# Kernel optimization log

Measured on AMD Instinct MI355X. Metric: run time of the kernel, lower is better.

Reference implementation:

```python
import jax, jax.numpy as jnp
import numpy as np

VAR_FLOOR = 0.002
BS, A, IN, H, L, NNH, ATT, NACT = 1024, 32, 96, 64, 16, 64, 32, 16


def _lin(x, w, b):
    return x @ w.T + b


def _lrelu(x):
    return jax.nn.leaky_relu(x, 0.01)


def setup_inputs() -> dict:
    key = jax.random.key(0)
    ks = jax.random.split(key, 24)
    def w(k, o, i):
        return jax.random.normal(k, (o, i), jnp.float32) / np.float32(np.sqrt(i))
    def b(k, o):
        return jax.random.normal(k, (o,), jnp.float32) * 0.01
    N = BS * A
    return {
        "inputs": jax.random.normal(ks[0], (N, IN), jnp.float32),
        "hidden_state": jax.random.normal(ks[1], (N, H), jnp.float32),
        "eps": jax.random.normal(ks[2], (N, A * L), jnp.float32),
        "fc1_w": w(ks[3], H, IN), "fc1_b": b(ks[4], H),
        "gru_wih": w(ks[5], 3 * H, H), "gru_whh": w(ks[6], 3 * H, H),
        "gru_bih": b(ks[7], 3 * H), "gru_bhh": b(ks[8], 3 * H),
        "fc2_w": w(ks[9], NACT, H), "fc2_b": b(ks[10], NACT),
        "emb_w1": w(ks[11], NNH, H), "emb_b1": b(ks[12], NNH),
        "bn_g": jnp.ones((NNH,), jnp.float32), "bn_b": jnp.zeros((NNH,), jnp.float32),
        "emb_w2": w(ks[13], A * L * 2, NNH), "emb_b2": b(ks[14], A * L * 2),
        "msg_w1": w(ks[15], NNH, H + L), "msg_b1": b(ks[16], NNH),
        "msg_w2": w(ks[17], NACT, NNH), "msg_b2": b(ks[18], NACT),
        "wq_w": w(ks[19], ATT, H), "wq_b": b(ks[20], ATT),
        "wk_w": w(ks[21], ATT, L), "wk_b": b(ks[22], ATT),
        "bs": BS, "t": 0,
    }


def reference(inputs, hidden_state, eps, fc1_w, fc1_b, gru_wih, gru_whh, gru_bih,
              gru_bhh, fc2_w, fc2_b, emb_w1, emb_b1, bn_g, bn_b, emb_w2, emb_b2,
              msg_w1, msg_b1, msg_w2, msg_b2, wq_w, wq_b, wk_w, wk_b, bs, t):
    Hd = fc1_w.shape[0]
    x = jax.nn.relu(_lin(inputs, fc1_w, fc1_b))
    h_in = hidden_state.reshape(-1, Hd)
    # GRUCell
    gi = _lin(x, gru_wih, gru_bih)
    gh = _lin(h_in, gru_whh, gru_bhh)
    ir, iz, inn = jnp.split(gi, 3, axis=-1)
    hr, hz, hn = jnp.split(gh, 3, axis=-1)
    r = jax.nn.sigmoid(ir + hr)
    z = jax.nn.sigmoid(iz + hz)
    n = jnp.tanh(inn + r * hn)
    h = (1.0 - z) * n + z * h_in
    q = _lin(h, fc2_w, fc2_b)
    # embed_net: Linear -> BatchNorm(train) -> LeakyReLU -> Linear
    z1 = _lin(h, emb_w1, emb_b1)
    z1 = bn_g * (z1 - z1.mean(0)) / jnp.sqrt(z1.var(0) + 1e-5) + bn_b
    lat_par = _lin(_lrelu(z1), emb_w2, emb_b2)
    D = lat_par.shape[-1] // 2
    Ld = wk_w.shape[1]
    Ag = D // Ld
    mu = lat_par[:, :D]
    var = jnp.clip(jnp.exp(lat_par[:, D:]), VAR_FLOOR, None)
    latent = (mu + jnp.sqrt(var) * eps).reshape(bs, Ag, Ag, Ld)  # [b,i,j,L]
    # msg_net on (h of receiver j, latent[b,i,j])
    h3 = h.reshape(bs, Ag, Hd)
    h_rep = jnp.broadcast_to(h3[:, None, :, :], (bs, Ag, Ag, Hd))  # [b,i,j]=h[b,j]
    msg_in = jnp.concatenate([h_rep, latent], axis=-1)
    msg = _lin(_lrelu(_lin(msg_in, msg_w1, msg_b1)), msg_w2, msg_b2)  # (b,A,A,n_act)
    # attention gating
    att = wq_w.shape[0]
    query = _lin(h, wq_w, wq_b).reshape(bs, Ag, att) / np.float32(np.sqrt(att))
    key_ = _lin(latent, wk_w, wk_b)  # (b,A,A,att)
    alpha = jnp.einsum('bia,bija->bij', query, key_)
    alpha = jnp.where(jnp.eye(Ag, dtype=bool)[None], -1e9, alpha)
    alpha = jax.nn.softmax(alpha, axis=-1)
    agg = jnp.einsum('bij,bijn->bjn', alpha, msg)  # sum gated msgs over sender i
    return_q = q + agg.reshape(bs * Ag, -1)
    return (return_q, h)
```

## Files before the change

### kernel.cpp

```cpp
#include <hip/hip_runtime.h>
#include <math.h>

namespace {

constexpr int NROW = 32768;
constexpr int HDIM = 64;
constexpr int DH   = 512;

typedef __attribute__((ext_vector_type(8))) short bf16x8;
typedef __attribute__((ext_vector_type(4))) float f32x4;
typedef __attribute__((ext_vector_type(4))) unsigned uint4e;
typedef __attribute__((ext_vector_type(2))) unsigned uint2e;

__device__ __forceinline__ float sigmoidf_(float x) { return 1.f / (1.f + __expf(-x)); }
__device__ __forceinline__ float lrelu_(float x) { return x > 0.f ? x : 0.01f * x; }
__device__ __forceinline__ unsigned pkbf(float a, float b) {
  unsigned ua = __float_as_uint(a) + 0x8000u;
  unsigned ub = __float_as_uint(b) + 0x8000u;
  return __builtin_amdgcn_perm(ub, ua, 0x07060302);
}

__global__ __launch_bounds__(512, 1) void k_fgru(
    const float* __restrict__ in,
    const float* __restrict__ hprev,
    const float* __restrict__ fc1w, const float* __restrict__ fc1b,
    const float* __restrict__ wih, const float* __restrict__ whh,
    const float* __restrict__ bih, const float* __restrict__ bhh,
    float* __restrict__ hT, float* __restrict__ hout) {
  __shared__ char smem[73728];
  const int t = threadIdx.x;
  const int n0 = blockIdx.x * 128;
  short*    xS = (short*)smem;
  unsigned* gU = (unsigned*)(smem + 18432);
  float*    trF = (float*)(smem + 18432);

  const float2* wih2 = (const float2*)wih;
  const float2* whh2 = (const float2*)whh;
  {
    float2 wv[12];
#pragma unroll
    for (int i = 0; i < 12; ++i) {
      int idx = t + 512 * i;
      int row = idx >> 5, kp = idx & 31;
      wv[i] = wih2[row * 32 + kp];
    }
#pragma unroll
    for (int i = 0; i < 12; ++i) {
      int idx = t + 512 * i;
      int row = idx >> 5, kp = idx & 31;
      int gate = row >> 6, cl = row & 63;
      gU[(gate * 64 + cl) * 36 + kp] = pkbf(wv[i].x, wv[i].y);
    }
#pragma unroll
    for (int i = 0; i < 12; ++i) {
      int idx = t + 512 * i;
      int row = idx >> 5, kp = idx & 31;
      wv[i] = whh2[row * 32 + kp];
    }
#pragma unroll
    for (int i = 0; i < 12; ++i) {
      int idx = t + 512 * i;
      int row = idx >> 5, kp = idx & 31;
      int gate = row >> 6, cl = row & 63;
      gU[((gate + 3) * 64 + cl) * 36 + kp] = pkbf(wv[i].x, wv[i].y);
    }
  }

  const int w = t >> 6, l = t & 63;
  const int m = l & 15, g = l >> 4;
  const int rowA = n0 + w * 16 + m;

  bf16x8 af[3];
#pragma unroll
  for (int ks = 0; ks < 3; ++ks) {
    const float4* p = (const float4*)(in + (size_t)rowA * 96 + ks * 32 + g * 8);
    float4 a = p[0], b = p[1];
    union { unsigned u[4]; bf16x8 h; } tw;
    tw.u[0] = pkbf(a.x, a.y); tw.u[1] = pkbf(a.z, a.w);
    tw.u[2] = pkbf(b.x, b.y); tw.u[3] = pkbf(b.z, b.w);
    af[ks] = tw.h;
  }
  {
    f32x4 accx[4];
#pragma unroll
    for (int ct = 0; ct < 4; ++ct) accx[ct] = (f32x4){0.f, 0.f, 0.f, 0.f};
#pragma unroll
    for (int ct = 0; ct < 4; ++ct)
#pragma unroll
      for (int ks = 0; ks < 3; ++ks) {
        const float4* p = (const float4*)(fc1w + (ct * 16 + m) * 96 + ks * 32 + g * 8);
        float4 a = p[0], b = p[1];
        union { unsigned u[4]; bf16x8 h; } tw;
        tw.u[0] = pkbf(a.x, a.y); tw.u[1] = pkbf(a.z, a.w);
        tw.u[2] = pkbf(b.x, b.y); tw.u[3] = pkbf(b.z, b.w);
        accx[ct] = __builtin_amdgcn_mfma_f32_16x16x32_bf16(af[ks], tw.h, accx[ct], 0, 0, 0);
      }
#pragma unroll
    for (int ct = 0; ct < 4; ++ct) {
      int c = ct * 16 + m;
      float bc = fc1b[c];
#pragma unroll
      for (int reg = 0; reg < 4; ++reg) {
        int nl = w * 16 + g * 4 + reg;
        float v = fmaxf(accx[ct][reg] + bc, 0.f);
        xS[nl * 72 + c] = (short)((__float_as_uint(v) + 0x8000u) >> 16);
      }
    }
  }
  __syncthreads();

  bf16x8 ax[2], ah[2];
#pragma unroll
  for (int ks = 0; ks < 2; ++ks) {
    ax[ks] = *(const bf16x8*)(xS + (w * 16 + m) * 72 + ks * 32 + g * 8);
    const float4* p = (const float4*)(hprev + (size_t)rowA * 64 + ks * 32 + g * 8);
    float4 a = p[0], b = p[1];
    union { unsigned u[4]; bf16x8 h; } tw;
    tw.u[0] = pkbf(a.x, a.y); tw.u[1] = pkbf(a.z, a.w);
    tw.u[2] = pkbf(b.x, b.y); tw.u[3] = pkbf(b.z, b.w);
    ah[ks] = tw.h;
  }
  const short* gS = (const short*)gU;
  float hc[4][4];
#pragma unroll 1
  for (int ct = 0; ct < 4; ++ct) {
    f32x4 a_ir = (f32x4){0.f,0.f,0.f,0.f}, a_iz = (f32x4){0.f,0.f,0.f,0.f},
          a_in = (f32x4){0.f,0.f,0.f,0.f}, a_hr = (f32x4){0.f,0.f,0.f,0.f},
          a_hz = (f32x4){0.f,0.f,0.f,0.f}, a_hn = (f32x4){0.f,0.f,0.f,0.f};
    int crow = ct * 16 + m;
#pragma unroll
    for (int ks = 0; ks < 2; ++ks) {
      bf16x8 b0 = *(const bf16x8*)(gS + (0 * 64 + crow) * 72 + ks * 32 + g * 8);
      bf16x8 b1 = *(const bf16x8*)(gS + (1 * 64 + crow) * 72 + ks * 32 + g * 8);
      bf16x8 b2 = *(const bf16x8*)(gS + (2 * 64 + crow) * 72 + ks * 32 + g * 8);
      bf16x8 b3 = *(const bf16x8*)(gS + (3 * 64 + crow) * 72 + ks * 32 + g * 8);
      bf16x8 b4 = *(const bf16x8*)(gS + (4 * 64 + crow) * 72 + ks * 32 + g * 8);
      bf16x8 b5 = *(const bf16x8*)(gS + (5 * 64 + crow) * 72 + ks * 32 + g * 8);
      a_ir = __builtin_amdgcn_mfma_f32_16x16x32_bf16(ax[ks], b0, a_ir, 0, 0, 0);
      a_iz = __builtin_amdgcn_mfma_f32_16x16x32_bf16(ax[ks], b1, a_iz, 0, 0, 0);
      a_in = __builtin_amdgcn_mfma_f32_16x16x32_bf16(ax[ks], b2, a_in, 0, 0, 0);
      a_hr = __builtin_amdgcn_mfma_f32_16x16x32_bf16(ah[ks], b3, a_hr, 0, 0, 0);
      a_hz = __builtin_amdgcn_mfma_f32_16x16x32_bf16(ah[ks], b4, a_hz, 0, 0, 0);
      a_hn = __builtin_amdgcn_mfma_f32_16x16x32_bf16(ah[ks], b5, a_hn, 0, 0, 0);
    }
    float bir = bih[crow], biz = bih[64 + crow], bin = bih[128 + crow];
    float bhr = bhh[crow], bhz = bhh[64 + crow], bhn = bhh[128 + crow];
#pragma unroll
    for (int reg = 0; reg < 4; ++reg) {
      int nl = w * 16 + g * 4 + reg;
      float hv = hprev[(size_t)(n0 + nl) * 64 + crow];
      float r  = sigmoidf_(a_ir[reg] + bir + a_hr[reg] + bhr);
      float z  = sigmoidf_(a_iz[reg] + biz + a_hz[reg] + bhz);
      float nn = tanhf(a_in[reg] + bin + r * (a_hn[reg] + bhn));
      hc[ct][reg] = (1.f - z) * nn + z * hv;
    }
  }
  __syncthreads();
#pragma unroll
  for (int ct = 0; ct < 4; ++ct)
#pragma unroll
    for (int reg = 0; reg < 4; ++reg)
      trF[(ct * 16 + m) * 133 + w * 16 + g * 4 + reg] = hc[ct][reg];
  __syncthreads();
#pragma unroll
  for (int i = 0; i < 16; ++i) {
    int idx = t + 512 * i;
    int nl = idx & 127, cl = idx >> 7;
    hT[(size_t)cl * NROW + n0 + nl] = trF[cl * 133 + nl];
  }
#pragma unroll
  for (int i = 0; i < 16; ++i) {
    int idx = t + 512 * i;
    int c = idx & 63, nl = idx >> 6;
    hout[(size_t)(n0 + nl) * 64 + c] = trF[c * 133 + nl];
  }
}

__global__ __launch_bounds__(256) void k_heads(const float* __restrict__ hT,
    const float* __restrict__ fc2w, const float* __restrict__ fc2b,
    const float* __restrict__ wqw, const float* __restrict__ wkw,
    const float* __restrict__ ew1, const float* __restrict__ eb1,
    float* __restrict__ qT, float* __restrict__ qkT, float* __restrict__ z1T,
    float* __restrict__ part) {
  __shared__ char smem[36864];
  const int t = threadIdx.x;
  const int n0 = blockIdx.x * 128;
  unsigned* hU = (unsigned*)smem;
  unsigned* wU = (unsigned*)(smem + 18432);
  float* sp1 = (float*)(smem + 18432 + 13824);
  float* sp2 = sp1 + 256;
  const float qs = 0.17677669529663687f;

  {
    float va[16], vb[16];
#pragma unroll
    for (int i = 0; i < 16; ++i) {
      int idx = t + 256 * i;
      int nl = idx & 127, kp = idx >> 7;
      va[i] = hT[(size_t)(2 * kp) * NROW + n0 + nl];
      vb[i] = hT[(size_t)(2 * kp + 1) * NROW + n0 + nl];
    }
#pragma unroll
    for (int i = 0; i < 16; ++i) {
      int idx = t + 256 * i;
      int nl = idx & 127, kp = idx >> 7;
      hU[nl * 36 + kp] = pkbf(va[i], vb[i]);
    }
  }
  {
    float2 wv[10];
#pragma unroll
    for (int i = 0; i < 10; ++i) {
      int idx = t + 256 * i;
      int kp = idx & 31, cl = idx >> 5;
      const float* src = (cl < 16) ? (fc2w + cl * 64) : (ew1 + (cl - 16) * 64);
      wv[i] = *(const float2*)(src + 2 * kp);
    }
#pragma unroll
    for (int i = 0; i < 10; ++i) {
      int idx = t + 256 * i;
      int kp = idx & 31, cl = idx >> 5;
      int dst = (cl < 16) ? cl : (cl + 16);
      wU[dst * 36 + kp] = pkbf(wv[i].x, wv[i].y);
    }
  }
  {
    int kp = t & 31, ll = t >> 5;
#pragma unroll
    for (int h = 0; h < 2; ++h) {
      int row = ll + 8 * h;
      float s0 = 0.f, s1 = 0.f;
#pragma unroll
      for (int a = 0; a < 32; ++a) {
        float wk = wkw[a * 16 + row];
        s0 = fmaf(wk, wqw[a * 64 + 2 * kp], s0);
        s1 = fmaf(wk, wqw[a * 64 + 2 * kp + 1], s1);
      }
      wU[(16 + row) * 36 + kp] = pkbf(s0 * qs, s1 * qs);
    }
  }
  __syncthreads();

  const int w = t >> 6, l = t & 63;
  const int m = l & 15, g = l >> 4;
  const short* sH = (const short*)hU;
  const short* sW = (const short*)wU;

  bf16x8 af[2][2];
#pragma unroll
  for (int mt = 0; mt < 2; ++mt)
#pragma unroll
    for (int ks = 0; ks < 2; ++ks)
      af[mt][ks] = *(const bf16x8*)(sH + (w * 32 + mt * 16 + m) * 72 + ks * 32 + g * 8);

  f32x4 acc[2][6];
#pragma unroll
  for (int mt = 0; mt < 2; ++mt)
#pragma unroll
    for (int ct = 0; ct < 6; ++ct) acc[mt][ct] = (f32x4){0.f, 0.f, 0.f, 0.f};
#pragma unroll
  for (int ct = 0; ct < 6; ++ct)
#pragma unroll
    for (int ks = 0; ks < 2; ++ks) {
      bf16x8 bw = *(const bf16x8*)(sW + (ct * 16 + m) * 72 + ks * 32 + g * 8);
#pragma unroll
      for (int mt = 0; mt < 2; ++mt)
        acc[mt][ct] = __builtin_amdgcn_mfma_f32_16x16x32_bf16(af[mt][ks], bw, acc[mt][ct], 0, 0, 0);
    }

  float s1[4], s2[4];
#pragma unroll
  for (int zt = 0; zt < 4; ++zt) { s1[zt] = 0.f; s2[zt] = 0.f; }
#pragma unroll
  for (int mt = 0; mt < 2; ++mt) {
    int nb = n0 + w * 32 + mt * 16 + g * 4;
    {
      float bc = fc2b[m];
      f32x4 v;
#pragma unroll
      for (int reg = 0; reg < 4; ++reg) v[reg] = acc[mt][0][reg] + bc;
      *(f32x4*)(qT + (size_t)m * NROW + nb) = v;
    }
    *(f32x4*)(qkT + (size_t)m * NROW + nb) = acc[mt][1];
#pragma unroll
    for (int ct = 2; ct < 6; ++ct) {
      int z = (ct - 2) * 16 + m;
      float bc = eb1[z];
      f32x4 v;
#pragma unroll
      for (int reg = 0; reg < 4; ++reg) {
        float zv = acc[mt][ct][reg] + bc;
        v[reg] = zv;
        s1[ct - 2] += zv;
        s2[ct - 2] = fmaf(zv, zv, s2[ct - 2]);
      }
      *(f32x4*)(z1T + (size_t)z * NROW + nb) = v;
    }
  }
#pragma unroll
  for (int zt = 0; zt < 4; ++zt) {
    s1[zt] += __shfl_down(s1[zt], 16, 64);
    s1[zt] += __shfl_down(s1[zt], 32, 64);
    s2[zt] += __shfl_down(s2[zt], 16, 64);
    s2[zt] += __shfl_down(s2[zt], 32, 64);
  }
  if (l < 16) {
#pragma unroll
    for (int zt = 0; zt < 4; ++zt) {
      sp1[w * 64 + zt * 16 + m] = s1[zt];
      sp2[w * 64 + zt * 16 + m] = s2[zt];
    }
  }
  __syncthreads();
  if (t < 64) {
    float a1 = sp1[t] + sp1[64 + t] + sp1[128 + t] + sp1[192 + t];
    float a2 = sp2[t] + sp2[64 + t] + sp2[128 + t] + sp2[192 + t];
    part[(size_t)blockIdx.x * 128 + t] = a1;
    part[(size_t)blockIdx.x * 128 + 64 + t] = a2;
  }
}

__global__ __launch_bounds__(256) void k_bnstat(const float* __restrict__ part,
    const float* __restrict__ bng, const float* __restrict__ bnb,
    const float* __restrict__ ew2,
    float* __restrict__ stat, unsigned* __restrict__ ew2b) {
  if (blockIdx.x == 0) {
    __shared__ float red[512];
    const int t = threadIdx.x;
    const int c = t & 63, q = t >> 6;
    float s1 = 0.f, s2 = 0.f;
#pragma unroll 4
    for (int b = q; b < 256; b += 4) {
      s1 += part[(size_t)b * 128 + c];
      s2 += part[(size_t)b * 128 + 64 + c];
    }
    red[q * 64 + c] = s1;
    red[256 + q * 64 + c] = s2;
    __syncthreads();
    if (t < 64) {
      float a1 = red[t] + red[64 + t] + red[128 + t] + red[192 + t];
      float a2 = red[256 + t] + red[320 + t] + red[384 + t] + red[448 + t];
      float mean = a1 * (1.f / NROW);
      float var = a2 * (1.f / NROW) - mean * mean;
      float rstd = rsqrtf(var + 1e-5f);
      float sc = bng[t] * rstd;
      stat[t] = sc;
      stat[64 + t] = bnb[t] - mean * sc;
    }
  } else {
    const int rb = blockIdx.x - 1;
    const int t = threadIdx.x;
#pragma unroll
    for (int it = 0; it < 2; ++it) {
      int id2 = t + 256 * it;
      int r = rb * 16 + (id2 >> 5);
      int cp = id2 & 31;
      float2 v = *(const float2*)(ew2 + (size_t)r * 64 + 2 * cp);
      ew2b[(size_t)r * 32 + cp] = pkbf(v.x, v.y);
    }
  }
}

constexpr int LATB_OFF = 0;
constexpr int H3B_OFF  = 40960;
constexpr int W1H_OFF  = 45568;
constexpr int W1L_OFF  = 54784;
constexpr int W2P_OFF  = 57344;
constexpr int ALL_OFF  = 59648;
constexpr int MT_OFF   = 63872;
constexpr int QKL_OFF  = 74112;
__global__ __launch_bounds__(256, 1) void k_msg(
    const unsigned* __restrict__ ew2b, const float* __restrict__ stat,
    const float* __restrict__ z1T, const float* __restrict__ eb2,
    const float* __restrict__ eps,
    const float* __restrict__ qkT,
    const float* __restrict__ qT, const float* __restrict__ hrow,
    const float* __restrict__ w1, const float* __restrict__ b1,
    const float* __restrict__ w2, const float* __restrict__ b2,
    float* __restrict__ out) {
  __shared__ char smem[76672];
  const int t = threadIdx.x;
  const int b = blockIdx.x;
  const int b32 = b * 32;
  unsigned* latB_dw = (unsigned*)(smem + LATB_OFF);

  const int w = t >> 6, l = t & 63;
  const int m = l & 15, g = l >> 4;

  {
    short* xz = (short*)(smem + MT_OFF);
    float zv[8];
#pragma unroll
    for (int it = 0; it < 8; ++it) {
      int idx = t + 256 * it;
      int i = idx & 31, c = idx >> 5;
      zv[it] = z1T[(size_t)c * NROW + b32 + i];
    }
#pragma unroll
    for (int it = 0; it < 8; ++it) {
      int idx = t + 256 * it;
      int i = idx & 31, c = idx >> 5;
      float v = lrelu_(fmaf(stat[c], zv[it], stat[64 + c]));
      xz[i * 72 + c] = (short)((__float_as_uint(v) + 0x8000u) >> 16);
    }
  }
  {
    float* qkL = (float*)(smem + QKL_OFF);
    int i = t & 31;
    float v0 = qkT[(size_t)((t >> 5)) * NROW + b32 + i];
    float v1 = qkT[(size_t)((t >> 5) + 8) * NROW + b32 + i];
    qkL[i * 20 + (t >> 5)] = v0;
    qkL[i * 20 + (t >> 5) + 8] = v1;
  }
  {
    int cp = t & 31, jj = t >> 5;
    const float2* h2 = (const float2*)hrow;
    float2 hv[4];
#pragma unroll
    for (int it = 0; it < 4; ++it)
      hv[it] = h2[((size_t)(b32 + jj + 8 * it) * 64 + 2 * cp) >> 1];
    unsigned* dst = (unsigned*)(smem + H3B_OFF);
#pragma unroll
    for (int it = 0; it < 4; ++it)
      dst[(jj + 8 * it) * 36 + cp] = pkbf(hv[it].x, hv[it].y);
  }
  {
    int kp = t & 31, cc = t >> 5;
    const float2* w12 = (const float2*)w1;
    float2 wv[8];
#pragma unroll
    for (int it = 0; it < 8; ++it)
      wv[it] = w12[((cc + 8 * it) * 80 + 2 * kp) >> 1];
    unsigned* dst = (unsigned*)(smem + W1H_OFF);
#pragma unroll
    for (int it = 0; it < 8; ++it)
      dst[(cc + 8 * it) * 36 + kp] = pkbf(wv[it].x, wv[it].y);
  }
  {
    int lp = t & 7, cc = t >> 3;
    const float2* w12 = (const float2*)w1;
    float2 wv[2];
#pragma unroll
    for (int it = 0; it < 2; ++it)
      wv[it] = w12[((cc + 32 * it) * 80 + 64 + 2 * lp) >> 1];
    unsigned* dst = (unsigned*)(smem + W1L_OFF);
#pragma unroll
    for (int it = 0; it < 2; ++it)
      dst[(cc + 32 * it) * 10 + lp] = pkbf(wv[it].x, wv[it].y);
  }
  {
    int pp = t & 31, nn = t >> 5;
    const float2* w22 = (const float2*)w2;
    int p = 2 * pp;
    int c = ((p >> 2) & 3) * 16 + (p >> 4) * 4 + (p & 3);
    float2 wv0 = w22[(nn * 64 + c) >> 1];
    float2 wv1 = w22[((nn + 8) * 64 + c) >> 1];
    unsigned* dst = (unsigned*)(smem + W2P_OFF);
    dst[nn * 36 + pp] = pkbf(wv0.x, wv0.y);
    dst[(nn + 8) * 36 + pp] = pkbf(wv1.x, wv1.y);
  }
  __syncthreads();

  {
    const short* xzS = (const short*)(smem + MT_OFF);
    bf16x8 afz[2][2];
#pragma unroll
    for (int mt = 0; mt < 2; ++mt)
#pragma unroll
      for (int ks = 0; ks < 2; ++ks)
        afz[mt][ks] = *(const bf16x8*)(xzS + (mt * 16 + m) * 72 + ks * 32 + g * 8);
    const uint4e* w4 = (const uint4e*)ew2b;
    const float stdfloor = 0.04472135955f;
#pragma unroll 2
    for (int ci8 = 0; ci8 < 8; ++ci8) {
      int ci = w * 8 + ci8;
      int c = ci * 16 + m;
      union { uint4e u; bf16x8 h; } bmu[2], blv[2];
#pragma unroll
      for (int ks = 0; ks < 2; ++ks) {
        bmu[ks].u = w4[(size_t)(ci * 16 + m) * 8 + ks * 4 + g];
        blv[ks].u = w4[(size_t)(512 + ci * 16 + m) * 8 + ks * 4 + g];
      }
      float ep[2][4];
#pragma unroll
      for (int mt = 0; mt < 2; ++mt)
#pragma unroll
        for (int reg = 0; reg < 4; ++reg)
          ep[mt][reg] = eps[(size_t)(b32 + mt * 16 + g * 4 + reg) * 512 + c];
      f32x4 accm[2], accl[2];
#pragma unroll
      for (int mt = 0; mt < 2; ++mt) {
        accm[mt] = (f32x4){0.f, 0.f, 0.f, 0.f};
        accl[mt] = (f32x4){0.f, 0.f, 0.f, 0.f};
      }
#pragma unroll
      for (int ks = 0; ks < 2; ++ks)
#pragma unroll
        for (int mt = 0; mt < 2; ++mt) {
          accm[mt] = __builtin_amdgcn_mfma_f32_16x16x32_bf16(afz[mt][ks], bmu[ks].h, accm[mt], 0, 0, 0);
          accl[mt] = __builtin_amdgcn_mfma_f32_16x16x32_bf16(afz[mt][ks], blv[ks].h, accl[mt], 0, 0, 0);
        }
      float ebm = eb2[c], ebl = eb2[DH + c];
#pragma unroll
      for (int mt = 0; mt < 2; ++mt)
#pragma unroll
        for (int reg = 0; reg < 4; ++reg) {
          float mu = accm[mt][reg] + ebm;
          float lv = accl[mt][reg] + ebl;
          float sd = fmaxf(__expf(0.5f * lv), stdfloor);
          float lat = fmaf(sd, ep[mt][reg], mu);
          float lat2 = __shfl_xor(lat, 1, 64);
          if (!(m & 1)) {
            int i = mt * 16 + g * 4 + reg;
            latB_dw[(i * 32 + ci) * 10 + (m >> 1)] = pkbf(lat, lat2);
          }
        }
    }
  }
  __syncthreads();

  {
    const float* qkL = (const float*)(smem + QKL_OFF);
    float* alL = (float*)(smem + ALL_OFF);
#pragma unroll 1
    for (int p = 0; p < 4; ++p) {
      int i = (t >> 5) + 8 * p;
      int j = t & 31;
      const unsigned* lr = latB_dw + (i * 32 + j) * 10;
      float acc = 0.f;
#pragma unroll
      for (int d = 0; d < 8; ++d) {
        unsigned u = lr[d];
        float lo = __uint_as_float(u << 16);
        float hi = __uint_as_float(u & 0xffff0000u);
        acc = fmaf(lo, qkL[i * 20 + 2 * d], acc);
        acc = fmaf(hi, qkL[i * 20 + 2 * d + 1], acc);
      }
      if (j == i) acc = -1e9f;
      float mx = acc;
#pragma unroll
      for (int msk = 16; msk > 0; msk >>= 1) mx = fmaxf(mx, __shfl_xor(mx, msk, 32));
      float e = __expf(acc - mx);
      float s = e;
#pragma unroll
      for (int msk = 16; msk > 0; msk >>= 1) s += __shfl_xor(s, msk, 32);
      alL[i * 33 + j] = e / s;
    }
  }

  const int n15 = l & 15, q = l >> 4;
  const int jh = w & 1, ibase = (w >> 1) * 16;
  const bool kact = (q < 2);

  f32x4 hp[4];
#pragma unroll
  for (int ct = 0; ct < 4; ++ct) hp[ct] = (f32x4){0.f, 0.f, 0.f, 0.f};
#pragma unroll
  for (int ct = 0; ct < 4; ++ct)
#pragma unroll
    for (int ks = 0; ks < 2; ++ks) {
      bf16x8 aF = *(const bf16x8*)(smem + W1H_OFF + (ct * 16 + n15) * 144 + ks * 64 + q * 16);
      bf16x8 bF = *(const bf16x8*)(smem + H3B_OFF + (jh * 16 + n15) * 144 + ks * 64 + q * 16);
      hp[ct] = __builtin_amdgcn_mfma_f32_16x16x32_bf16(aF, bF, hp[ct], 0, 0, 0);
    }
#pragma unroll
  for (int ct = 0; ct < 4; ++ct)
#pragma unroll
    for (int reg = 0; reg < 4; ++reg)
      hp[ct][reg] += b1[ct * 16 + q * 4 + reg];

  bf16x8 aL[4];
#pragma unroll
  for (int ct = 0; ct < 4; ++ct) {
    union { unsigned u[4]; bf16x8 h; } tmp;
    tmp.u[0] = tmp.u[1] = tmp.u[2] = tmp.u[3] = 0u;
    if (kact) {
      const unsigned* p = (const unsigned*)(smem + W1L_OFF) + (ct * 16 + n15) * 10 + q * 4;
      uint2e d0 = *(const uint2e*)p;
      uint2e d1 = *(const uint2e*)(p + 2);
      tmp.u[0] = d0.x; tmp.u[1] = d0.y; tmp.u[2] = d1.x; tmp.u[3] = d1.y;
    }
    aL[ct] = tmp.h;
  }
  bf16x8 w2F[2];
#pragma unroll
  for (int ks = 0; ks < 2; ++ks)
    w2F[ks] = *(const bf16x8*)(smem + W2P_OFF + n15 * 144 + ks * 64 + q * 16);
  float b2v[4];
#pragma unroll
  for (int reg = 0; reg < 4; ++reg) b2v[reg] = b2[q * 4 + reg];

  __syncthreads();

  float agg[4] = {0.f, 0.f, 0.f, 0.f};
  char* wb = smem + MT_OFF + w * 2560;
  const float* alLf = (const float*)(smem + ALL_OFF);
#pragma unroll 1
  for (int it = 0; it < 16; ++it) {
    int ii = ibase + it;
    int r = ii * 32 + jh * 16 + n15;
    union { unsigned u[4]; bf16x8 h; } latF;
    latF.u[0] = latF.u[1] = latF.u[2] = latF.u[3] = 0u;
    if (kact) {
      const unsigned* p = latB_dw + r * 10 + q * 4;
      uint2e d0 = *(const uint2e*)p;
      uint2e d1 = *(const uint2e*)(p + 2);
      latF.u[0] = d0.x; latF.u[1] = d0.y; latF.u[2] = d1.x; latF.u[3] = d1.y;
    }
    f32x4 acc[4];
#pragma unroll
    for (int ct = 0; ct < 4; ++ct) {
      acc[ct] = (f32x4){0.f, 0.f, 0.f, 0.f};
      acc[ct] = __builtin_amdgcn_mfma_f32_16x16x32_bf16(aL[ct], latF.h, acc[ct], 0, 0, 0);
    }
#pragma unroll
    for (int h = 0; h < 2; ++h) {
      float m0[4], m1[4];
#pragma unroll
      for (int reg = 0; reg < 4; ++reg) {
        float v0 = acc[2 * h][reg] + hp[2 * h][reg];
        float v1 = acc[2 * h + 1][reg] + hp[2 * h + 1][reg];
        m0[reg] = fmaxf(v0, 0.01f * v0);
        m1[reg] = fmaxf(v1, 0.01f * v1);
      }
      uint4e pk4;
      pk4.x = pkbf(m0[0], m0[1]); pk4.y = pkbf(m0[2], m0[3]);
      pk4.z = pkbf(m1[0], m1[1]); pk4.w = pkbf(m1[2], m1[3]);
      int qp = (2 * q + h) & 3;
      *(uint4e*)(wb + (q >> 1) * 1280 + n15 * 80 + qp * 16) = pk4;
    }
    f32x4 msg = (f32x4){0.f, 0.f, 0.f, 0.f};
#pragma unroll
    for (int ks = 0; ks < 2; ++ks) {
      bf16x8 mF = *(const bf16x8*)(wb + ks * 1280 + n15 * 80 + q * 16);
      msg = __builtin_amdgcn_mfma_f32_16x16x32_bf16(w2F[ks], mF, msg, 0, 0, 0);
    }
    float aw = alLf[ii * 33 + jh * 16 + n15];
#pragma unroll
    for (int reg = 0; reg < 4; ++reg)
      agg[reg] = fmaf(aw, msg[reg] + b2v[reg], agg[reg]);
  }
  {
    f32x4 av; av[0] = agg[0]; av[1] = agg[1]; av[2] = agg[2]; av[3] = agg[3];
    *(f32x4*)(wb + n15 * 80 + q * 16) = av;
  }
  __syncthreads();
#pragma unroll
  for (int tt = 0; tt < 2; ++tt) {
    int idx = t + 256 * tt;
    int jg = idx >> 4, nn = idx & 15;
    int jh2 = jg >> 4, jl = jg & 15;
    float a0 = *(const float*)(smem + MT_OFF + jh2 * 2560 + jl * 80 + nn * 4);
    float a1 = *(const float*)(smem + MT_OFF + (jh2 + 2) * 2560 + jl * 80 + nn * 4);
    out[(size_t)b * 512 + idx] = a0 + a1 + qT[(size_t)nn * NROW + b32 + jg];
  }
}

}

extern "C" void kernel_launch(void* const* d_in, const int* in_sizes, int n_in,
                              void* d_out, int out_size, void* d_ws, size_t ws_size,
                              hipStream_t stream) {
  (void)in_sizes; (void)n_in; (void)out_size; (void)ws_size;
  const float* inputs = (const float*)d_in[0];
  const float* hidden = (const float*)d_in[1];
  const float* eps    = (const float*)d_in[2];
  const float* fc1w   = (const float*)d_in[3];
  const float* fc1b   = (const float*)d_in[4];
  const float* wih    = (const float*)d_in[5];
  const float* whh    = (const float*)d_in[6];
  const float* bih    = (const float*)d_in[7];
  const float* bhh    = (const float*)d_in[8];
  const float* fc2w   = (const float*)d_in[9];
  const float* fc2b   = (const float*)d_in[10];
  const float* ew1    = (const float*)d_in[11];
  const float* eb1    = (const float*)d_in[12];
  const float* bng    = (const float*)d_in[13];
  const float* bnb    = (const float*)d_in[14];
  const float* ew2    = (const float*)d_in[15];
  const float* eb2    = (const float*)d_in[16];
  const float* w1     = (const float*)d_in[17];
  const float* b1     = (const float*)d_in[18];
  const float* w2     = (const float*)d_in[19];
  const float* b2     = (const float*)d_in[20];
  const float* wqw    = (const float*)d_in[21];
  const float* wkw    = (const float*)d_in[23];

  float* ws = (float*)d_ws;
  float* hT     = ws;
  float* qT     = ws + 2097152;
  float* qkT    = ws + 2621440;
  float* z1T    = ws + 3670016;
  float* part   = ws + 5767168;
  float* stat   = ws + 5832704;
  unsigned* ew2b = (unsigned*)(ws + 5832832);

  float* out_q = (float*)d_out;
  float* out_h = (float*)d_out + 524288;

  hipLaunchKernelGGL(k_fgru, dim3(256), dim3(512), 0, stream,
                     inputs, hidden, fc1w, fc1b, wih, whh, bih, bhh, hT, out_h);
  hipLaunchKernelGGL(k_heads, dim3(256), dim3(256), 0, stream,
                     hT, fc2w, fc2b, wqw, wkw, ew1, eb1, qT, qkT, z1T, part);
  hipLaunchKernelGGL(k_bnstat, dim3(65), dim3(256), 0, stream, part, bng, bnb, ew2, stat, ew2b);
  hipLaunchKernelGGL(k_msg, dim3(1024), dim3(256), 0, stream,
                     ew2b, stat, z1T, eb2, eps, qkT, qT, out_h, w1, b1, w2, b2, out_q);
}
```

Measured before the change: 238.7 us.

## Run message kernel with 512 threads per block and a tighter latent LDS stride

```diff
diff --git a/kernel.cpp b/kernel.cpp
--- a/kernel.cpp
+++ b/kernel.cpp
@@ -362,14 +362,14 @@
 }
 
 constexpr int LATB_OFF = 0;
-constexpr int H3B_OFF  = 40960;
-constexpr int W1H_OFF  = 45568;
-constexpr int W1L_OFF  = 54784;
-constexpr int W2P_OFF  = 57344;
-constexpr int ALL_OFF  = 59648;
-constexpr int MT_OFF   = 63872;
-constexpr int QKL_OFF  = 74112;
-__global__ __launch_bounds__(256, 1) void k_msg(
+constexpr int H3B_OFF  = 36864;
+constexpr int W1H_OFF  = 41472;
+constexpr int W1L_OFF  = 50688;
+constexpr int W2P_OFF  = 53248;
+constexpr int ALL_OFF  = 55552;
+constexpr int MT_OFF   = 59776;
+constexpr int QKL_OFF  = MT_OFF + 4608;
+__global__ __launch_bounds__(512, 1) void k_msg(
     const unsigned* __restrict__ ew2b, const float* __restrict__ stat,
     const float* __restrict__ z1T, const float* __restrict__ eb2,
     const float* __restrict__ eps,
@@ -378,7 +378,7 @@
     const float* __restrict__ w1, const float* __restrict__ b1,
     const float* __restrict__ w2, const float* __restrict__ b2,
     float* __restrict__ out) {
-  __shared__ char smem[76672];
+  __shared__ char smem[80256];
   const int t = threadIdx.x;
   const int b = blockIdx.x;
   const int b32 = b * 32;
@@ -389,16 +389,16 @@
 
   {
     short* xz = (short*)(smem + MT_OFF);
-    float zv[8];
-#pragma unroll
-    for (int it = 0; it < 8; ++it) {
-      int idx = t + 256 * it;
+    float zv[4];
+#pragma unroll
+    for (int it = 0; it < 4; ++it) {
+      int idx = t + 512 * it;
       int i = idx & 31, c = idx >> 5;
       zv[it] = z1T[(size_t)c * NROW + b32 + i];
     }
 #pragma unroll
-    for (int it = 0; it < 8; ++it) {
-      int idx = t + 256 * it;
+    for (int it = 0; it < 4; ++it) {
+      int idx = t + 512 * it;
       int i = idx & 31, c = idx >> 5;
       float v = lrelu_(fmaf(stat[c], zv[it], stat[64 + c]));
       xz[i * 72 + c] = (short)((__float_as_uint(v) + 0x8000u) >> 16);
@@ -406,47 +406,39 @@
   }
   {
     float* qkL = (float*)(smem + QKL_OFF);
-    int i = t & 31;
-    float v0 = qkT[(size_t)((t >> 5)) * NROW + b32 + i];
-    float v1 = qkT[(size_t)((t >> 5) + 8) * NROW + b32 + i];
-    qkL[i * 20 + (t >> 5)] = v0;
-    qkL[i * 20 + (t >> 5) + 8] = v1;
-  }
-  {
-    int cp = t & 31, jj = t >> 5;
+    int i = t & 31, ll = t >> 5;
+    qkL[i * 20 + ll] = qkT[(size_t)ll * NROW + b32 + i];
+  }
+  {
+    int cp = t & 31, jbase = t >> 5;
     const float2* h2 = (const float2*)hrow;
-    float2 hv[4];
+    float2 hv[2];
+#pragma unroll
+    for (int it = 0; it < 2; ++it)
+      hv[it] = h2[((size_t)(b32 + jbase + 16 * it) * 64 + 2 * cp) >> 1];
+    unsigned* dst = (unsigned*)(smem + H3B_OFF);
+#pragma unroll
+    for (int it = 0; it < 2; ++it)
+      dst[(jbase + 16 * it) * 36 + cp] = pkbf(hv[it].x, hv[it].y);
+  }
+  {
+    int kp = t & 31, cb = t >> 5;
+    const float2* w12 = (const float2*)w1;
+    float2 wv[4];
 #pragma unroll
     for (int it = 0; it < 4; ++it)
-      hv[it] = h2[((size_t)(b32 + jj + 8 * it) * 64 + 2 * cp) >> 1];
-    unsigned* dst = (unsigned*)(smem + H3B_OFF);
+      wv[it] = w12[((cb + 16 * it) * 80 + 2 * kp) >> 1];
+    unsigned* dst = (unsigned*)(smem + W1H_OFF);
 #pragma unroll
     for (int it = 0; it < 4; ++it)
-      dst[(jj + 8 * it) * 36 + cp] = pkbf(hv[it].x, hv[it].y);
-  }
-  {
-    int kp = t & 31, cc = t >> 5;
-    const float2* w12 = (const float2*)w1;
-    float2 wv[8];
-#pragma unroll
-    for (int it = 0; it < 8; ++it)
-      wv[it] = w12[((cc + 8 * it) * 80 + 2 * kp) >> 1];
-    unsigned* dst = (unsigned*)(smem + W1H_OFF);
-#pragma unroll
-    for (int it = 0; it < 8; ++it)
-      dst[(cc + 8 * it) * 36 + kp] = pkbf(wv[it].x, wv[it].y);
+      dst[(cb + 16 * it) * 36 + kp] = pkbf(wv[it].x, wv[it].y);
   }
   {
     int lp = t & 7, cc = t >> 3;
     const float2* w12 = (const float2*)w1;
-    float2 wv[2];
-#pragma unroll
-    for (int it = 0; it < 2; ++it)
-      wv[it] = w12[((cc + 32 * it) * 80 + 64 + 2 * lp) >> 1];
+    float2 wv = w12[(cc * 80 + 64 + 2 * lp) >> 1];
     unsigned* dst = (unsigned*)(smem + W1L_OFF);
-#pragma unroll
-    for (int it = 0; it < 2; ++it)
-      dst[(cc + 32 * it) * 10 + lp] = pkbf(wv[it].x, wv[it].y);
+    dst[cc * 10 + lp] = pkbf(wv.x, wv.y);
   }
   {
     int pp = t & 31, nn = t >> 5;
@@ -454,10 +446,8 @@
     int p = 2 * pp;
     int c = ((p >> 2) & 3) * 16 + (p >> 4) * 4 + (p & 3);
     float2 wv0 = w22[(nn * 64 + c) >> 1];
-    float2 wv1 = w22[((nn + 8) * 64 + c) >> 1];
     unsigned* dst = (unsigned*)(smem + W2P_OFF);
     dst[nn * 36 + pp] = pkbf(wv0.x, wv0.y);
-    dst[(nn + 8) * 36 + pp] = pkbf(wv1.x, wv1.y);
   }
   __syncthreads();
 
@@ -472,8 +462,8 @@
     const uint4e* w4 = (const uint4e*)ew2b;
     const float stdfloor = 0.04472135955f;
 #pragma unroll 2
-    for (int ci8 = 0; ci8 < 8; ++ci8) {
-      int ci = w * 8 + ci8;
+    for (int ci8 = 0; ci8 < 4; ++ci8) {
+      int ci = w * 4 + ci8;
       int c = ci * 16 + m;
       union { uint4e u; bf16x8 h; } bmu[2], blv[2];
 #pragma unroll
@@ -512,7 +502,7 @@
           float lat2 = __shfl_xor(lat, 1, 64);
           if (!(m & 1)) {
             int i = mt * 16 + g * 4 + reg;
-            latB_dw[(i * 32 + ci) * 10 + (m >> 1)] = pkbf(lat, lat2);
+            latB_dw[(i * 32 + ci) * 9 + (m >> 1)] = pkbf(lat, lat2);
           }
         }
     }
@@ -523,10 +513,10 @@
     const float* qkL = (const float*)(smem + QKL_OFF);
     float* alL = (float*)(smem + ALL_OFF);
 #pragma unroll 1
-    for (int p = 0; p < 4; ++p) {
-      int i = (t >> 5) + 8 * p;
+    for (int p = 0; p < 2; ++p) {
+      int i = (t >> 5) + 16 * p;
       int j = t & 31;
-      const unsigned* lr = latB_dw + (i * 32 + j) * 10;
+      const unsigned* lr = latB_dw + (i * 32 + j) * 9;
       float acc = 0.f;
 #pragma unroll
       for (int d = 0; d < 8; ++d) {
@@ -549,7 +539,7 @@
   }
 
   const int n15 = l & 15, q = l >> 4;
-  const int jh = w & 1, ibase = (w >> 1) * 16;
+  const int jh = w & 1, ibase = (w >> 1) * 8;
   const bool kact = (q < 2);
 
   f32x4 hp[4];
@@ -596,16 +586,14 @@
   char* wb = smem + MT_OFF + w * 2560;
   const float* alLf = (const float*)(smem + ALL_OFF);
 #pragma unroll 1
-  for (int it = 0; it < 16; ++it) {
+  for (int it = 0; it < 8; ++it) {
     int ii = ibase + it;
     int r = ii * 32 + jh * 16 + n15;
     union { unsigned u[4]; bf16x8 h; } latF;
     latF.u[0] = latF.u[1] = latF.u[2] = latF.u[3] = 0u;
     if (kact) {
-      const unsigned* p = latB_dw + r * 10 + q * 4;
-      uint2e d0 = *(const uint2e*)p;
-      uint2e d1 = *(const uint2e*)(p + 2);
-      latF.u[0] = d0.x; latF.u[1] = d0.y; latF.u[2] = d1.x; latF.u[3] = d1.y;
+      const unsigned* p = latB_dw + r * 9 + q * 4;
+      latF.u[0] = p[0]; latF.u[1] = p[1]; latF.u[2] = p[2]; latF.u[3] = p[3];
     }
     f32x4 acc[4];
 #pragma unroll
@@ -645,14 +633,14 @@
     *(f32x4*)(wb + n15 * 80 + q * 16) = av;
   }
   __syncthreads();
-#pragma unroll
-  for (int tt = 0; tt < 2; ++tt) {
-    int idx = t + 256 * tt;
-    int jg = idx >> 4, nn = idx & 15;
+  {
+    int jg = t >> 4, nn = t & 15;
     int jh2 = jg >> 4, jl = jg & 15;
-    float a0 = *(const float*)(smem + MT_OFF + jh2 * 2560 + jl * 80 + nn * 4);
-    float a1 = *(const float*)(smem + MT_OFF + (jh2 + 2) * 2560 + jl * 80 + nn * 4);
-    out[(size_t)b * 512 + idx] = a0 + a1 + qT[(size_t)nn * NROW + b32 + jg];
+    float s = qT[(size_t)nn * NROW + b32 + jg];
+#pragma unroll
+    for (int k = 0; k < 4; ++k)
+      s += *(const float*)(smem + MT_OFF + (jh2 + 2 * k) * 2560 + jl * 80 + nn * 4);
+    out[(size_t)b * 512 + t] = s;
   }
 }
 
@@ -703,6 +691,6 @@
   hipLaunchKernelGGL(k_heads, dim3(256), dim3(256), 0, stream,
                      hT, fc2w, fc2b, wqw, wkw, ew1, eb1, qT, qkT, z1T, part);
   hipLaunchKernelGGL(k_bnstat, dim3(65), dim3(256), 0, stream, part, bng, bnb, ew2, stat, ew2b);
-  hipLaunchKernelGGL(k_msg, dim3(1024), dim3(256), 0, stream,
+  hipLaunchKernelGGL(k_msg, dim3(1024), dim3(512), 0, stream,
                      ew2b, stat, z1T, eb2, eps, qkT, qT, out_h, w1, b1, w2, b2, out_q);
 }
```

Result: faster. 227.4 us (-4.8%).
